# Optimization experiments

Measured on AMD Instinct MI355X. Metric: run time of the kernel, lower is better.

Reference implementation:

```python
import jax, jax.numpy as jnp
import numpy as np

N_NODES = 50000
N_EDGES = 800000
D_FEAT = 128
K_HOPS = 2


def setup_inputs() -> dict:
    key = jax.random.key(0)
    k1, k2, k3 = jax.random.split(key, 3)
    features = jax.random.normal(k1, (N_NODES, D_FEAT), dtype=jnp.float32)
    src = jax.random.randint(k2, (N_EDGES,), 0, N_NODES, dtype=jnp.int64)
    dst = jax.random.randint(k3, (N_EDGES,), 0, N_NODES, dtype=jnp.int64)
    return {"features": features, "src": src, "dst": dst}


def reference(features, src, dst):
    """SGCLayer: k=2 hops, degree-normalized copy_u/sum aggregation, mean layer aggr."""
    n = features.shape[0]
    # in_degrees: number of incoming edges per node, clamped to >= 1
    deg = jax.ops.segment_sum(jnp.ones(dst.shape, dtype=features.dtype), dst,
                              num_segments=n)
    norm = jnp.power(jnp.clip(deg, 1.0), -0.5)[:, None]  # [N, 1]
    h = features
    results = [features]
    for _ in range(K_HOPS):
        h = h * norm                   # pre-scale by D^-1/2
        m = h[src]                     # copy_u: gather source features [E, F]
        h = jax.ops.segment_sum(m, dst, num_segments=n)  # sum into dst [N, F]
        h = h * norm                   # post-scale by D^-1/2
        results.append(h)
    # layer_aggr == 'mean': average over the k+1 propagated representations
    H = jnp.stack(results, axis=1)     # [N, k+1, F]
    return jnp.mean(H, axis=1)
```

## Files before the change

kernel.cpp:

```cpp
#include <hip/hip_runtime.h>

#define N_NODES 50000
#define N_EDGES 800000
#define D_FEAT  128
#define ELL_CAP 64
#define NRANGE  49
#define NALIAS  64
#define ALIAS_MASK 63
#define SCAP    384
#define NBLK_A  782

typedef unsigned int uint;
typedef unsigned short ushort_t;

union f32u { float f; uint u; };

__device__ __forceinline__ ushort_t f2bf(float f) {
    f32u x; x.f = f;
    uint u = x.u;
    return (ushort_t)((u + 0x7FFFu + ((u >> 16) & 1u)) >> 16);
}

__global__ void zero_gcnt(int* __restrict__ gcnt) {
    int i = blockIdx.x * 256 + threadIdx.x;
    if (i < NRANGE * NALIAS) gcnt[i] = 0;
}

__global__ __launch_bounds__(256) void bucketize(const int4* __restrict__ dst4,
                                                 const int4* __restrict__ src4,
                                                 int* __restrict__ gcnt,
                                                 uint* __restrict__ stage) {
    __shared__ int lcnt[NRANGE];
    __shared__ int lbase[NRANGE];
    int tid = threadIdx.x;
    int g = blockIdx.x;
    for (int i = tid; i < NRANGE; i += 256) lcnt[i] = 0;
    __syncthreads();
    int i4 = g * 256 + tid;
    bool valid = (i4 < N_EDGES / 4);
    int4 d4 = valid ? dst4[i4] : make_int4(0, 0, 0, 0);
    int4 s4 = valid ? src4[i4] : make_int4(0, 0, 0, 0);
    int r0 = 0, r1 = 0, r2 = 0, r3 = 0, k0 = 0, k1 = 0, k2 = 0, k3 = 0;
    if (valid) {
        r0 = d4.x >> 10; k0 = atomicAdd(&lcnt[r0], 1);
        r1 = d4.y >> 10; k1 = atomicAdd(&lcnt[r1], 1);
        r2 = d4.z >> 10; k2 = atomicAdd(&lcnt[r2], 1);
        r3 = d4.w >> 10; k3 = atomicAdd(&lcnt[r3], 1);
    }
    __syncthreads();
    int alias = g & ALIAS_MASK;
    if (tid < NRANGE) {
        int c = lcnt[tid];
        lbase[tid] = c ? atomicAdd(&gcnt[tid * NALIAS + alias], c) : 0;
    }
    __syncthreads();
    if (valid) {
        int b;
        b = lbase[r0] + k0;
        if (b < SCAP) stage[(r0 * NALIAS + alias) * SCAP + b] =
            ((uint)(d4.x & 1023) << 16) | (uint)s4.x;
        b = lbase[r1] + k1;
        if (b < SCAP) stage[(r1 * NALIAS + alias) * SCAP + b] =
            ((uint)(d4.y & 1023) << 16) | (uint)s4.y;
        b = lbase[r2] + k2;
        if (b < SCAP) stage[(r2 * NALIAS + alias) * SCAP + b] =
            ((uint)(d4.z & 1023) << 16) | (uint)s4.z;
        b = lbase[r3] + k3;
        if (b < SCAP) stage[(r3 * NALIAS + alias) * SCAP + b] =
            ((uint)(d4.w & 1023) << 16) | (uint)s4.w;
    }
}

__global__ __launch_bounds__(1024) void rank_build(const int* __restrict__ gcnt,
                                                   const uint* __restrict__ stage,
                                                   int* __restrict__ ell,
                                                   int* __restrict__ cnt,
                                                   float* __restrict__ norm) {
    __shared__ int hist[1024];
    __shared__ int rc[NALIAS];
    __shared__ int pfx[NALIAS + 1];
    int r = blockIdx.x;
    int tid = threadIdx.x;
    hist[tid] = 0;
    if (tid < NALIAS) {
        int n = gcnt[r * NALIAS + tid];
        rc[tid] = n > SCAP ? SCAP : n;
    }
    __syncthreads();
    if (tid == 0) {
        int run = 0;
        for (int a = 0; a < NALIAS; a++) { pfx[a] = run; run += rc[a]; }
        pfx[NALIAS] = run;
    }
    __syncthreads();
    int T = pfx[NALIAS];
    for (int j = tid; j < T; j += 1024) {
        int loa = 0, hia = NALIAS;
        while (hia - loa > 1) {
            int mid = (loa + hia) >> 1;
            if (pfx[mid] <= j) loa = mid; else hia = mid;
        }
        uint v = stage[(r * NALIAS + loa) * SCAP + (j - pfx[loa])];
        int ld = v >> 16;
        int s = (int)(v & 0xFFFFu);
        int p = atomicAdd(&hist[ld], 1);
        if (p < ELL_CAP) ell[(((r << 10) + ld) << 6) + p] = s;
    }
    __syncthreads();
    int node = (r << 10) + tid;
    if (node < N_NODES) {
        int c = hist[tid];
        cnt[node] = c;
        norm[node] = rsqrtf((float)(c < 1 ? 1 : c));
    }
}

__global__ void convert_scale(const float4* __restrict__ feat4,
                              const float* __restrict__ norm,
                              ushort4* __restrict__ featb4) {
    int gid = blockIdx.x * 256 + threadIdx.x;
    if (gid < N_NODES * (D_FEAT / 4)) {
        float nn = norm[gid >> 5];
        float4 v = feat4[gid];
        ushort4 o;
        o.x = f2bf(v.x * nn); o.y = f2bf(v.y * nn);
        o.z = f2bf(v.z * nn); o.w = f2bf(v.w * nn);
        featb4[gid] = o;
    }
}

template<int FINAL>
__global__ void hop_gather(const int* __restrict__ ell, const int* __restrict__ cnt,
                           const ushort_t* __restrict__ hb, const float* __restrict__ norm,
                           const float* __restrict__ feat, const ushort_t* __restrict__ s1,
                           void* __restrict__ outp) {
    int node = blockIdx.x * 4 + (threadIdx.x >> 6);
    int lane = threadIdx.x & 63;
    int q    = lane >> 4;
    int l16  = lane & 15;
    const uint4* hbv = (const uint4*)hb;
    int b    = node * ELL_CAP;
    int ecnt = cnt[node];
    if (ecnt > ELL_CAP) ecnt = ELL_CAP;
    float a0 = 0, a1 = 0, a2 = 0, a3 = 0, a4 = 0, a5 = 0, a6 = 0, a7 = 0;

#define ACC2(P, E_, O_) { f32u lo_, hi_; lo_.u = (P) << 16; hi_.u = (P) & 0xFFFF0000u; \
                          E_ += lo_.f; O_ += hi_.f; }
#define ACCV(V) { ACC2(V.x, a0, a1); ACC2(V.y, a2, a3); ACC2(V.z, a4, a5); ACC2(V.w, a6, a7); }

    int i = 0;
    for (; i + 16 <= ecnt; i += 16) {
        int s0 = ell[b + i      + q];
        int s1i = ell[b + i + 4  + q];
        int s2 = ell[b + i + 8  + q];
        int s3 = ell[b + i + 12 + q];
        uint4 v0 = hbv[s0 * 16 + l16];
        uint4 v1 = hbv[s1i * 16 + l16];
        uint4 v2 = hbv[s2 * 16 + l16];
        uint4 v3 = hbv[s3 * 16 + l16];
        ACCV(v0); ACCV(v1); ACCV(v2); ACCV(v3);
    }
    if (i + 8 <= ecnt) {
        int s0 = ell[b + i     + q];
        int s1i = ell[b + i + 4 + q];
        uint4 v0 = hbv[s0 * 16 + l16];
        uint4 v1 = hbv[s1i * 16 + l16];
        ACCV(v0); ACCV(v1);
        i += 8;
    }
    if (i + 4 <= ecnt) {
        int s_ = ell[b + i + q];
        uint4 v_ = hbv[s_ * 16 + l16];
        ACCV(v_);
        i += 4;
    }
    int rem = ecnt - i;
    if (q < rem) {
        int s_ = ell[b + i + q];
        uint4 v_ = hbv[s_ * 16 + l16];
        ACCV(v_);
    }
#undef ACCV
#undef ACC2

    a0 += __shfl_xor(a0, 16, 64); a1 += __shfl_xor(a1, 16, 64);
    a2 += __shfl_xor(a2, 16, 64); a3 += __shfl_xor(a3, 16, 64);
    a4 += __shfl_xor(a4, 16, 64); a5 += __shfl_xor(a5, 16, 64);
    a6 += __shfl_xor(a6, 16, 64); a7 += __shfl_xor(a7, 16, 64);
    a0 += __shfl_xor(a0, 32, 64); a1 += __shfl_xor(a1, 32, 64);
    a2 += __shfl_xor(a2, 32, 64); a3 += __shfl_xor(a3, 32, 64);
    a4 += __shfl_xor(a4, 32, 64); a5 += __shfl_xor(a5, 32, 64);
    a6 += __shfl_xor(a6, 32, 64); a7 += __shfl_xor(a7, 32, 64);

    if (q == 0) {
        float nn = norm[node];
        if (!FINAL) {
            float n2 = nn * nn;
            uint4 o;
            o.x = (uint)f2bf(a0 * n2) | ((uint)f2bf(a1 * n2) << 16);
            o.y = (uint)f2bf(a2 * n2) | ((uint)f2bf(a3 * n2) << 16);
            o.z = (uint)f2bf(a4 * n2) | ((uint)f2bf(a5 * n2) << 16);
            o.w = (uint)f2bf(a6 * n2) | ((uint)f2bf(a7 * n2) << 16);
            ((uint4*)outp)[node * 16 + l16] = o;
        } else {
            float inv = 1.0f / nn;
            uint4 p = ((const uint4*)s1)[node * 16 + l16];
            f32u t0, t1, t2, t3, t4, t5, t6, t7;
            t0.u = p.x << 16; t1.u = p.x & 0xFFFF0000u;
            t2.u = p.y << 16; t3.u = p.y & 0xFFFF0000u;
            t4.u = p.z << 16; t5.u = p.z & 0xFFFF0000u;
            t6.u = p.w << 16; t7.u = p.w & 0xFFFF0000u;
            const float4* f4 = (const float4*)feat;
            float4 fA = f4[node * 32 + 2 * l16];
            float4 fB = f4[node * 32 + 2 * l16 + 1];
            const float third = 1.0f / 3.0f;
            float4 rA, rB;
            rA.x = (fA.x + t0.f * inv + nn * a0) * third;
            rA.y = (fA.y + t1.f * inv + nn * a1) * third;
            rA.z = (fA.z + t2.f * inv + nn * a2) * third;
            rA.w = (fA.w + t3.f * inv + nn * a3) * third;
            rB.x = (fB.x + t4.f * inv + nn * a4) * third;
            rB.y = (fB.y + t5.f * inv + nn * a5) * third;
            rB.z = (fB.z + t6.f * inv + nn * a6) * third;
            rB.w = (fB.w + t7.f * inv + nn * a7) * third;
            ((float4*)outp)[node * 32 + 2 * l16]     = rA;
            ((float4*)outp)[node * 32 + 2 * l16 + 1] = rB;
        }
    }
}

extern "C" void kernel_launch(void* const* d_in, const int* in_sizes, int n_in,
                              void* d_out, int out_size, void* d_ws, size_t ws_size,
                              hipStream_t stream) {
    const float* feat = (const float*)d_in[0];
    const int*   src  = (const int*)d_in[1];
    const int*   dst  = (const int*)d_in[2];
    float* out = (float*)d_out;

    char* ws = (char*)d_ws;
    int*      gcnt  = (int*)     (ws + 0x0000000);
    int*      cnt   = (int*)     (ws + 0x0010000);
    float*    norm  = (float*)   (ws + 0x0050000);
    uint*     stage = (uint*)    (ws + 0x0090000);
    int*      ell   = (int*)     (ws + 0x0530000);
    ushort_t* featb = (ushort_t*)(ws + 0x1200000);
    ushort_t* s1b   = (ushort_t*)(ws + 0x1F00000);

    zero_gcnt<<<(NRANGE * NALIAS + 255) / 256, 256, 0, stream>>>(gcnt);
    bucketize<<<NBLK_A, 256, 0, stream>>>((const int4*)dst, (const int4*)src,
                                          gcnt, stage);
    rank_build<<<NRANGE, 1024, 0, stream>>>(gcnt, stage, ell, cnt, norm);
    convert_scale<<<(N_NODES * (D_FEAT / 4) + 255) / 256, 256, 0, stream>>>(
        (const float4*)feat, norm, (ushort4*)featb);

    hop_gather<0><<<N_NODES / 4, 256, 0, stream>>>(ell, cnt, featb, norm,
                                                   nullptr, nullptr, s1b);
    hop_gather<1><<<N_NODES / 4, 256, 0, stream>>>(ell, cnt, s1b, norm,
                                                   feat, s1b, out);
}
```

Before: 105.3 us.

## Split bf16 features into column-group slices and gather per slice

Stores the bf16 scaled features in 8 column-group slices of 32 bytes per node, laid out slice-major. The hop kernels now assign each block a single column group across 16 nodes, so the gathers for a given slice hit a 3.2 MB working set. The intent is better L2/cache locality for the random source-row gathers. ELL indices shrink to 16-bit, which halves the index traffic. The trade-off is that each node's neighbor list is now read 8 times (once per slice), the loads become narrower, and the shuffle reduction is longer.

```diff
diff --git a/kernel.cpp b/kernel.cpp
--- a/kernel.cpp
+++ b/kernel.cpp
@@ -9,6 +9,7 @@
 #define ALIAS_MASK 63
 #define SCAP    384
 #define NBLK_A  782
+#define NCG     8
 
 typedef unsigned int uint;
 typedef unsigned short ushort_t;
@@ -73,7 +74,7 @@
 
 __global__ __launch_bounds__(1024) void rank_build(const int* __restrict__ gcnt,
                                                    const uint* __restrict__ stage,
-                                                   int* __restrict__ ell,
+                                                   ushort_t* __restrict__ ell,
                                                    int* __restrict__ cnt,
                                                    float* __restrict__ norm) {
     __shared__ int hist[1024];
@@ -102,9 +103,9 @@
         }
         uint v = stage[(r * NALIAS + loa) * SCAP + (j - pfx[loa])];
         int ld = v >> 16;
-        int s = (int)(v & 0xFFFFu);
         int p = atomicAdd(&hist[ld], 1);
-        if (p < ELL_CAP) ell[(((r << 10) + ld) << 6) + p] = s;
+        if (p < ELL_CAP)
+            ell[(((r << 10) + ld) << 6) + p] = (ushort_t)(v & 0xFFFFu);
     }
     __syncthreads();
     int node = (r << 10) + tid;
@@ -115,84 +116,70 @@
     }
 }
 
-__global__ void convert_scale(const float4* __restrict__ feat4,
-                              const float* __restrict__ norm,
-                              ushort4* __restrict__ featb4) {
-    int gid = blockIdx.x * 256 + threadIdx.x;
-    if (gid < N_NODES * (D_FEAT / 4)) {
-        float nn = norm[gid >> 5];
-        float4 v = feat4[gid];
-        ushort4 o;
-        o.x = f2bf(v.x * nn); o.y = f2bf(v.y * nn);
-        o.z = f2bf(v.z * nn); o.w = f2bf(v.w * nn);
-        featb4[gid] = o;
+__global__ void convert_cg(const float4* __restrict__ feat4,
+                           const float* __restrict__ norm,
+                           uint4* __restrict__ featb_cg) {
+    int j = blockIdx.x * 256 + threadIdx.x;
+    if (j < N_NODES * NCG) {
+        int node = j >> 3, g = j & 7;
+        float nn = norm[node];
+        const float4* fp = feat4 + node * 32 + g * 4;
+        float4 f0 = fp[0], f1 = fp[1], f2 = fp[2], f3 = fp[3];
+        uint4 oA, oB;
+        oA.x = (uint)f2bf(f0.x * nn) | ((uint)f2bf(f0.y * nn) << 16);
+        oA.y = (uint)f2bf(f0.z * nn) | ((uint)f2bf(f0.w * nn) << 16);
+        oA.z = (uint)f2bf(f1.x * nn) | ((uint)f2bf(f1.y * nn) << 16);
+        oA.w = (uint)f2bf(f1.z * nn) | ((uint)f2bf(f1.w * nn) << 16);
+        oB.x = (uint)f2bf(f2.x * nn) | ((uint)f2bf(f2.y * nn) << 16);
+        oB.y = (uint)f2bf(f2.z * nn) | ((uint)f2bf(f2.w * nn) << 16);
+        oB.z = (uint)f2bf(f3.x * nn) | ((uint)f2bf(f3.y * nn) << 16);
+        oB.w = (uint)f2bf(f3.z * nn) | ((uint)f2bf(f3.w * nn) << 16);
+        uint4* op = featb_cg + (size_t)(g * N_NODES + node) * 2;
+        op[0] = oA; op[1] = oB;
     }
 }
 
 template<int FINAL>
-__global__ void hop_gather(const int* __restrict__ ell, const int* __restrict__ cnt,
-                           const ushort_t* __restrict__ hb, const float* __restrict__ norm,
-                           const float* __restrict__ feat, const ushort_t* __restrict__ s1,
-                           void* __restrict__ outp) {
-    int node = blockIdx.x * 4 + (threadIdx.x >> 6);
-    int lane = threadIdx.x & 63;
-    int q    = lane >> 4;
-    int l16  = lane & 15;
-    const uint4* hbv = (const uint4*)hb;
-    int b    = node * ELL_CAP;
+__global__ __launch_bounds__(256) void hop_cg(const ushort_t* __restrict__ ell,
+                                              const int* __restrict__ cnt,
+                                              const uint4* __restrict__ hb_cg,
+                                              const float* __restrict__ norm,
+                                              const float4* __restrict__ feat4,
+                                              const uint4* __restrict__ s1_cg,
+                                              void* __restrict__ outp) {
+    int cg    = blockIdx.x & 7;
+    int nbase = (blockIdx.x >> 3) * 16;
+    int wave  = threadIdx.x >> 6;
+    int lane  = threadIdx.x & 63;
+    int sub   = lane & 15;
+    int node  = nbase + wave * 4 + (lane >> 4);
+    int half  = sub & 1;
+    int eslot = sub >> 1;
     int ecnt = cnt[node];
     if (ecnt > ELL_CAP) ecnt = ELL_CAP;
+    int b = node * ELL_CAP;
+    int slice = cg * N_NODES;
     float a0 = 0, a1 = 0, a2 = 0, a3 = 0, a4 = 0, a5 = 0, a6 = 0, a7 = 0;
 
 #define ACC2(P, E_, O_) { f32u lo_, hi_; lo_.u = (P) << 16; hi_.u = (P) & 0xFFFF0000u; \
                           E_ += lo_.f; O_ += hi_.f; }
-#define ACCV(V) { ACC2(V.x, a0, a1); ACC2(V.y, a2, a3); ACC2(V.z, a4, a5); ACC2(V.w, a6, a7); }
-
-    int i = 0;
-    for (; i + 16 <= ecnt; i += 16) {
-        int s0 = ell[b + i      + q];
-        int s1i = ell[b + i + 4  + q];
-        int s2 = ell[b + i + 8  + q];
-        int s3 = ell[b + i + 12 + q];
-        uint4 v0 = hbv[s0 * 16 + l16];
-        uint4 v1 = hbv[s1i * 16 + l16];
-        uint4 v2 = hbv[s2 * 16 + l16];
-        uint4 v3 = hbv[s3 * 16 + l16];
-        ACCV(v0); ACCV(v1); ACCV(v2); ACCV(v3);
-    }
-    if (i + 8 <= ecnt) {
-        int s0 = ell[b + i     + q];
-        int s1i = ell[b + i + 4 + q];
-        uint4 v0 = hbv[s0 * 16 + l16];
-        uint4 v1 = hbv[s1i * 16 + l16];
-        ACCV(v0); ACCV(v1);
-        i += 8;
-    }
-    if (i + 4 <= ecnt) {
-        int s_ = ell[b + i + q];
-        uint4 v_ = hbv[s_ * 16 + l16];
-        ACCV(v_);
-        i += 4;
-    }
-    int rem = ecnt - i;
-    if (q < rem) {
-        int s_ = ell[b + i + q];
-        uint4 v_ = hbv[s_ * 16 + l16];
-        ACCV(v_);
-    }
-#undef ACCV
+    for (int i = eslot; i < ecnt; i += 8) {
+        int s = (int)ell[b + i];
+        uint4 v = hb_cg[(size_t)(slice + s) * 2 + half];
+        ACC2(v.x, a0, a1); ACC2(v.y, a2, a3);
+        ACC2(v.z, a4, a5); ACC2(v.w, a6, a7);
+    }
 #undef ACC2
 
-    a0 += __shfl_xor(a0, 16, 64); a1 += __shfl_xor(a1, 16, 64);
-    a2 += __shfl_xor(a2, 16, 64); a3 += __shfl_xor(a3, 16, 64);
-    a4 += __shfl_xor(a4, 16, 64); a5 += __shfl_xor(a5, 16, 64);
-    a6 += __shfl_xor(a6, 16, 64); a7 += __shfl_xor(a7, 16, 64);
-    a0 += __shfl_xor(a0, 32, 64); a1 += __shfl_xor(a1, 32, 64);
-    a2 += __shfl_xor(a2, 32, 64); a3 += __shfl_xor(a3, 32, 64);
-    a4 += __shfl_xor(a4, 32, 64); a5 += __shfl_xor(a5, 32, 64);
-    a6 += __shfl_xor(a6, 32, 64); a7 += __shfl_xor(a7, 32, 64);
-
-    if (q == 0) {
+#pragma unroll
+    for (int o = 2; o <= 8; o <<= 1) {
+        a0 += __shfl_xor(a0, o, 64); a1 += __shfl_xor(a1, o, 64);
+        a2 += __shfl_xor(a2, o, 64); a3 += __shfl_xor(a3, o, 64);
+        a4 += __shfl_xor(a4, o, 64); a5 += __shfl_xor(a5, o, 64);
+        a6 += __shfl_xor(a6, o, 64); a7 += __shfl_xor(a7, o, 64);
+    }
+
+    if (sub < 2) {
         float nn = norm[node];
         if (!FINAL) {
             float n2 = nn * nn;
@@ -201,18 +188,17 @@
             o.y = (uint)f2bf(a2 * n2) | ((uint)f2bf(a3 * n2) << 16);
             o.z = (uint)f2bf(a4 * n2) | ((uint)f2bf(a5 * n2) << 16);
             o.w = (uint)f2bf(a6 * n2) | ((uint)f2bf(a7 * n2) << 16);
-            ((uint4*)outp)[node * 16 + l16] = o;
+            ((uint4*)outp)[(size_t)(slice + node) * 2 + half] = o;
         } else {
             float inv = 1.0f / nn;
-            uint4 p = ((const uint4*)s1)[node * 16 + l16];
+            uint4 p = s1_cg[(size_t)(slice + node) * 2 + half];
             f32u t0, t1, t2, t3, t4, t5, t6, t7;
             t0.u = p.x << 16; t1.u = p.x & 0xFFFF0000u;
             t2.u = p.y << 16; t3.u = p.y & 0xFFFF0000u;
             t4.u = p.z << 16; t5.u = p.z & 0xFFFF0000u;
             t6.u = p.w << 16; t7.u = p.w & 0xFFFF0000u;
-            const float4* f4 = (const float4*)feat;
-            float4 fA = f4[node * 32 + 2 * l16];
-            float4 fB = f4[node * 32 + 2 * l16 + 1];
+            const float4* fp = feat4 + node * 32 + cg * 4 + half * 2;
+            float4 fA = fp[0], fB = fp[1];
             const float third = 1.0f / 3.0f;
             float4 rA, rB;
             rA.x = (fA.x + t0.f * inv + nn * a0) * third;
@@ -223,8 +209,8 @@
             rB.y = (fB.y + t5.f * inv + nn * a5) * third;
             rB.z = (fB.z + t6.f * inv + nn * a6) * third;
             rB.w = (fB.w + t7.f * inv + nn * a7) * third;
-            ((float4*)outp)[node * 32 + 2 * l16]     = rA;
-            ((float4*)outp)[node * 32 + 2 * l16 + 1] = rB;
+            float4* op = (float4*)outp + node * 32 + cg * 4 + half * 2;
+            op[0] = rA; op[1] = rB;
         }
     }
 }
@@ -242,19 +228,20 @@
     int*      cnt   = (int*)     (ws + 0x0010000);
     float*    norm  = (float*)   (ws + 0x0050000);
     uint*     stage = (uint*)    (ws + 0x0090000);
-    int*      ell   = (int*)     (ws + 0x0530000);
-    ushort_t* featb = (ushort_t*)(ws + 0x1200000);
-    ushort_t* s1b   = (ushort_t*)(ws + 0x1F00000);
+    ushort_t* ell   = (ushort_t*)(ws + 0x0530000);
+    uint4*    featb = (uint4*)   (ws + 0x0C00000);
+    uint4*    s1b   = (uint4*)   (ws + 0x1900000);
 
     zero_gcnt<<<(NRANGE * NALIAS + 255) / 256, 256, 0, stream>>>(gcnt);
     bucketize<<<NBLK_A, 256, 0, stream>>>((const int4*)dst, (const int4*)src,
                                           gcnt, stage);
     rank_build<<<NRANGE, 1024, 0, stream>>>(gcnt, stage, ell, cnt, norm);
-    convert_scale<<<(N_NODES * (D_FEAT / 4) + 255) / 256, 256, 0, stream>>>(
-        (const float4*)feat, norm, (ushort4*)featb);
-
-    hop_gather<0><<<N_NODES / 4, 256, 0, stream>>>(ell, cnt, featb, norm,
-                                                   nullptr, nullptr, s1b);
-    hop_gather<1><<<N_NODES / 4, 256, 0, stream>>>(ell, cnt, s1b, norm,
-                                                   feat, s1b, out);
-}
+    convert_cg<<<(N_NODES * NCG + 255) / 256, 256, 0, stream>>>(
+        (const float4*)feat, norm, featb);
+
+    const int hop_blocks = (N_NODES / 16) * NCG;
+    hop_cg<0><<<hop_blocks, 256, 0, stream>>>(ell, cnt, featb, norm,
+                                              (const float4*)feat, nullptr, s1b);
+    hop_cg<1><<<hop_blocks, 256, 0, stream>>>(ell, cnt, s1b, norm,
+                                              (const float4*)feat, s1b, out);
+}
```

Result: slower. 136.0 us (+29.1%).
